# Optimization experiments

Measured on AMD Instinct MI355X. Metric: run time of the kernel, lower is better.

## Reference

```python
import jax, jax.numpy as jnp
import numpy as np

D = 512      # n_embd
H = 8        # n_head
L = 2        # n_layer (per stack)
T = 2048     # sequence length / block_size
B = 1        # batch
BANDS = (999, 9)  # band_width for [phase, tool] stacks
EPS = 1e-5


def _sinusoidal(n_pos, dim):
    pos = np.arange(n_pos)[:, None].astype(np.float64)
    j = np.arange(dim)[None, :]
    angle = pos / np.power(10000.0, 2 * (j // 2) / dim)
    out = np.zeros((n_pos, dim), np.float32)
    out[:, 0::2] = np.sin(angle[:, 0::2])
    out[:, 1::2] = np.cos(angle[:, 1::2])
    return jnp.asarray(out)


def setup_inputs() -> dict:
    key = jax.random.key(0)
    ks = jax.random.split(key, 8)
    s = 0.02
    rn = lambda k, shp: jax.random.normal(k, shp, jnp.float32) * s
    inp = {
        "x": jax.random.normal(ks[0], (B, T, D), jnp.float32),
        "pos_emb": _sinusoidal(T, D),            # sinusoidal, frozen
        # leading dim 2 = [phase stack, tool stack], then layer dim L
        "ln1_w": jnp.ones((2, L, D)), "ln1_b": jnp.zeros((2, L, D)),
        "ln2_w": jnp.ones((2, L, D)), "ln2_b": jnp.zeros((2, L, D)),
        "Wq": rn(ks[1], (2, L, D, D)), "bq": jnp.zeros((2, L, D)),
        "Wk": rn(ks[2], (2, L, D, D)), "bk": jnp.zeros((2, L, D)),
        "Wv": rn(ks[3], (2, L, D, D)), "bv": jnp.zeros((2, L, D)),
        "Wo": rn(ks[4], (2, L, D, D)), "bo": jnp.zeros((2, L, D)),
        "W1": rn(ks[5], (2, L, D, 2 * D)), "b1": jnp.zeros((2, L, 2 * D)),
        "W2": rn(ks[6], (2, L, 2 * D, D)), "b2": jnp.zeros((2, L, D)),
        "lnf_w": jnp.ones((D,)), "lnf_b": jnp.zeros((D,)),
    }
    return inp


def _ln(x, w, b):
    mu = x.mean(-1, keepdims=True)
    var = ((x - mu) ** 2).mean(-1, keepdims=True)
    return (x - mu) / jnp.sqrt(var + EPS) * w + b


def _attn(x, Wq, bq, Wk, bk, Wv, bv, Wo, bo, bw):
    Bx, Tx, _ = x.shape
    Dh = D // H
    heads = lambda W, b: (x @ W + b).reshape(Bx, Tx, H, Dh).transpose(0, 2, 1, 3)
    q, k, v = heads(Wq, bq), heads(Wk, bk), heads(Wv, bv)
    att = jnp.einsum('bhqd,bhkd->bhqk', q, k) / jnp.sqrt(jnp.float32(Dh))
    i = jnp.arange(Tx)[:, None]
    j = jnp.arange(Tx)[None, :]
    mask = (j <= i) & (j >= i - bw)  # causal band
    att = jnp.where(mask, att, -jnp.inf)
    att = jax.nn.softmax(att, axis=-1)
    y = jnp.einsum('bhqk,bhkd->bhqd', att, v).transpose(0, 2, 1, 3).reshape(Bx, Tx, D)
    return y @ Wo + bo


def reference(x, pos_emb, ln1_w, ln1_b, ln2_w, ln2_b,
              Wq, bq, Wk, bk, Wv, bv, Wo, bo,
              W1, b1, W2, b2, lnf_w, lnf_b):
    Tx = x.shape[1]
    h0 = x + pos_emb[None, :Tx]
    outs = []
    for s in range(2):  # phase stack, tool stack
        bw = BANDS[s]
        h = h0
        for l in range(L):
            h = h + _attn(_ln(h, ln1_w[s, l], ln1_b[s, l]),
                          Wq[s, l], bq[s, l], Wk[s, l], bk[s, l],
                          Wv[s, l], bv[s, l], Wo[s, l], bo[s, l], bw)
            hm = _ln(h, ln2_w[s, l], ln2_b[s, l])
            h = h + (jax.nn.gelu(hm @ W1[s, l] + b1[s, l], approximate=False)
                     @ W2[s, l] + b2[s, l])
        outs.append(_ln(h, lnf_w, lnf_b))
    return (outs[0], outs[1])
```

## Files before the change

### kernel.cpp

```cpp
#include <hip/hip_runtime.h>
#include <stdint.h>

#define T 2048
#define D 512
#define NH 8
#define DH 64
#define L 2

typedef float floatx4 __attribute__((ext_vector_type(4)));
typedef short shortx8 __attribute__((ext_vector_type(8)));
typedef unsigned short u16;
typedef unsigned short u16x4 __attribute__((ext_vector_type(4)));

__device__ __forceinline__ u16 f2bf(float f) {
    union { float f; uint32_t u; } c; c.f = f;
    uint32_t u = c.u;
    u += 0x7fffu + ((u >> 16) & 1u);
    return (u16)(u >> 16);
}

__device__ __forceinline__ float bf2f(u16 v) {
    union { uint32_t u; float f; } c; c.u = ((uint32_t)v) << 16;
    return c.f;
}

__device__ __forceinline__ void load_lds16(const void* g, void* l) {
    __builtin_amdgcn_global_load_lds((const __attribute__((address_space(1))) void*)g,
                                     (__attribute__((address_space(3))) void*)l,
                                     16, 0, 0);
}

struct TransJobs {
    const float* src[6];
    u16* dst[6];
    const float* x;
    const float* pos;
    u16* h;
};

__global__ __launch_bounds__(256) void pre_kernel(TransJobs j) {
    __shared__ float tile[32][33];
    int tid = threadIdx.x;
    if (blockIdx.z == 24) {
        int idx = (blockIdx.y * 32 + blockIdx.x) * 256 + tid;
        float4 xv = ((const float4*)j.x)[idx];
        float4 pv = ((const float4*)j.pos)[idx];
        u16x4 hh;
        hh[0] = f2bf(xv.x + pv.x); hh[1] = f2bf(xv.y + pv.y);
        hh[2] = f2bf(xv.z + pv.z); hh[3] = f2bf(xv.w + pv.w);
        ((u16x4*)j.h)[idx] = hh;
        ((u16x4*)j.h)[idx + (T * D / 4)] = hh;
        return;
    }
    int m = blockIdx.z >> 2, slice = blockIdx.z & 3;
    int R = (m == 5) ? 1024 : 512;
    int C = (m == 4) ? 1024 : 512;
    if (blockIdx.x * 32 >= C || blockIdx.y * 32 >= R) return;
    const float* in = j.src[m] + (size_t)slice * R * C;
    u16* out = j.dst[m] + (size_t)slice * R * C;
    int tx = tid & 31, ty = tid >> 5;
    int x = blockIdx.x * 32 + tx;
    int y0 = blockIdx.y * 32;
#pragma unroll
    for (int i = 0; i < 4; i++)
        tile[ty + i * 8][tx] = in[(size_t)(y0 + ty + i * 8) * C + x];
    __syncthreads();
    int ox = y0 + tx;
#pragma unroll
    for (int i = 0; i < 4; i++)
        out[(size_t)(blockIdx.x * 32 + ty + i * 8) * R + ox] = f2bf(tile[tx][ty + i * 8]);
}

__global__ __launch_bounds__(256) void ln_res_kernel(u16* __restrict__ h,
                                                     const u16* __restrict__ part,
                                                     const float* __restrict__ wp,
                                                     const float* __restrict__ bp,
                                                     u16* __restrict__ out, int l) {
    int row = blockIdx.x * 4 + (threadIdx.x >> 6);
    int lane = threadIdx.x & 63;
    int s = row >> 11;
    int c0 = lane * 4;
    u16* xr = h + (size_t)row * D;
    u16x4 h0 = *(const u16x4*)(xr + c0);
    u16x4 h1 = *(const u16x4*)(xr + c0 + 256);
    float4 v0, v1;
    v0.x = bf2f(h0[0]); v0.y = bf2f(h0[1]); v0.z = bf2f(h0[2]); v0.w = bf2f(h0[3]);
    v1.x = bf2f(h1[0]); v1.y = bf2f(h1[1]); v1.z = bf2f(h1[2]); v1.w = bf2f(h1[3]);
    if (part) {
        const u16* p0r = part + (size_t)s * 2 * T * D + (size_t)(row & (T - 1)) * D;
        const u16* p1r = p0r + (size_t)T * D;
        u16x4 a0 = *(const u16x4*)(p0r + c0), a1 = *(const u16x4*)(p0r + c0 + 256);
        u16x4 e0 = *(const u16x4*)(p1r + c0), e1 = *(const u16x4*)(p1r + c0 + 256);
        v0.x += bf2f(a0[0]) + bf2f(e0[0]); v0.y += bf2f(a0[1]) + bf2f(e0[1]);
        v0.z += bf2f(a0[2]) + bf2f(e0[2]); v0.w += bf2f(a0[3]) + bf2f(e0[3]);
        v1.x += bf2f(a1[0]) + bf2f(e1[0]); v1.y += bf2f(a1[1]) + bf2f(e1[1]);
        v1.z += bf2f(a1[2]) + bf2f(e1[2]); v1.w += bf2f(a1[3]) + bf2f(e1[3]);
        u16x4 s0, s1;
        s0[0] = f2bf(v0.x); s0[1] = f2bf(v0.y); s0[2] = f2bf(v0.z); s0[3] = f2bf(v0.w);
        s1[0] = f2bf(v1.x); s1[1] = f2bf(v1.y); s1[2] = f2bf(v1.z); s1[3] = f2bf(v1.w);
        *(u16x4*)(xr + c0) = s0;
        *(u16x4*)(xr + c0 + 256) = s1;
    }
    float sum = v0.x + v0.y + v0.z + v0.w + v1.x + v1.y + v1.z + v1.w;
    float sq = v0.x*v0.x + v0.y*v0.y + v0.z*v0.z + v0.w*v0.w
             + v1.x*v1.x + v1.y*v1.y + v1.z*v1.z + v1.w*v1.w;
#pragma unroll
    for (int d2 = 1; d2 < 64; d2 <<= 1) { sum += __shfl_xor(sum, d2); sq += __shfl_xor(sq, d2); }
    float mu = sum * (1.0f / D);
    float var = sq * (1.0f / D) - mu * mu;
    float rstd = rsqrtf(var + 1e-5f);
    const float* w = wp + (size_t)(s * L + l) * D;
    const float* b = bp + (size_t)(s * L + l) * D;
    u16x4 p0, p1;
#pragma unroll
    for (int jj = 0; jj < 4; jj++) {
        float a = (jj == 0 ? v0.x : jj == 1 ? v0.y : jj == 2 ? v0.z : v0.w);
        p0[jj] = f2bf((a - mu) * rstd * w[c0 + jj] + b[c0 + jj]);
        float c = (jj == 0 ? v1.x : jj == 1 ? v1.y : jj == 2 ? v1.z : v1.w);
        p1[jj] = f2bf((c - mu) * rstd * w[c0 + 256 + jj] + b[c0 + 256 + jj]);
    }
    *(u16x4*)(out + (size_t)row * D + c0) = p0;
    *(u16x4*)(out + (size_t)row * D + c0 + 256) = p1;
}

__global__ __launch_bounds__(256) void lnf_kernel(const u16* __restrict__ h,
                                                  const u16* __restrict__ part,
                                                  const float* __restrict__ w,
                                                  const float* __restrict__ b,
                                                  float* __restrict__ out) {
    int row = blockIdx.x * 4 + (threadIdx.x >> 6);
    int lane = threadIdx.x & 63;
    int s = row >> 11;
    int c0 = lane * 4;
    const u16* xr = h + (size_t)row * D;
    u16x4 h0 = *(const u16x4*)(xr + c0);
    u16x4 h1 = *(const u16x4*)(xr + c0 + 256);
    float4 v0, v1;
    v0.x = bf2f(h0[0]); v0.y = bf2f(h0[1]); v0.z = bf2f(h0[2]); v0.w = bf2f(h0[3]);
    v1.x = bf2f(h1[0]); v1.y = bf2f(h1[1]); v1.z = bf2f(h1[2]); v1.w = bf2f(h1[3]);
    const u16* p0r = part + (size_t)s * 2 * T * D + (size_t)(row & (T - 1)) * D;
    const u16* p1r = p0r + (size_t)T * D;
    u16x4 a0 = *(const u16x4*)(p0r + c0), a1 = *(const u16x4*)(p0r + c0 + 256);
    u16x4 e0 = *(const u16x4*)(p1r + c0), e1 = *(const u16x4*)(p1r + c0 + 256);
    v0.x += bf2f(a0[0]) + bf2f(e0[0]); v0.y += bf2f(a0[1]) + bf2f(e0[1]);
    v0.z += bf2f(a0[2]) + bf2f(e0[2]); v0.w += bf2f(a0[3]) + bf2f(e0[3]);
    v1.x += bf2f(a1[0]) + bf2f(e1[0]); v1.y += bf2f(a1[1]) + bf2f(e1[1]);
    v1.z += bf2f(a1[2]) + bf2f(e1[2]); v1.w += bf2f(a1[3]) + bf2f(e1[3]);
    float sum = v0.x + v0.y + v0.z + v0.w + v1.x + v1.y + v1.z + v1.w;
    float sq = v0.x*v0.x + v0.y*v0.y + v0.z*v0.z + v0.w*v0.w
             + v1.x*v1.x + v1.y*v1.y + v1.z*v1.z + v1.w*v1.w;
#pragma unroll
    for (int d2 = 1; d2 < 64; d2 <<= 1) { sum += __shfl_xor(sum, d2); sq += __shfl_xor(sq, d2); }
    float mu = sum * (1.0f / D);
    float var = sq * (1.0f / D) - mu * mu;
    float rstd = rsqrtf(var + 1e-5f);
    float4 r0, r1;
    r0.x = (v0.x - mu) * rstd * w[c0+0] + b[c0+0];
    r0.y = (v0.y - mu) * rstd * w[c0+1] + b[c0+1];
    r0.z = (v0.z - mu) * rstd * w[c0+2] + b[c0+2];
    r0.w = (v0.w - mu) * rstd * w[c0+3] + b[c0+3];
    r1.x = (v1.x - mu) * rstd * w[c0+256+0] + b[c0+256+0];
    r1.y = (v1.y - mu) * rstd * w[c0+256+1] + b[c0+256+1];
    r1.z = (v1.z - mu) * rstd * w[c0+256+2] + b[c0+256+2];
    r1.w = (v1.w - mu) * rstd * w[c0+256+3] + b[c0+256+3];
    *(float4*)(out + (size_t)row * D + c0) = r0;
    *(float4*)(out + (size_t)row * D + c0 + 256) = r1;
}

struct GemmPtrs {
    const u16* A[6];
    const u16* Bt[6];
    const float* bias[6];
    void* C[6];
};

#define EPI_QKV  0
#define EPI_GELU 1
#define EPI_PART 2

template <int EPI>
__global__ __launch_bounds__(256) void gemm_kernel(GemmPtrs p, int M, int N, int K, int KS) {
    __shared__ __align__(16) u16 lA[2][64 * 32];
    __shared__ __align__(16) u16 lB[2][64 * 32];
    int nchunk = K / KS;
    int pidx = blockIdx.z / nchunk;
    int kc = blockIdx.z % nchunk;
    int koff = kc * KS;
    const u16* A = p.A[pidx];
    const u16* Bt = p.Bt[pidx];
    int m0 = blockIdx.y * 64, n0 = blockIdx.x * 64;
    int tid = threadIdx.x;
    int lane = tid & 63, wave = tid >> 6;
    int wx = wave & 1, wy = wave >> 1;
    int l16 = lane & 15, q4 = lane >> 4;
    const u16* ag = A + (size_t)(m0 + (tid >> 2)) * K + koff + (tid & 3) * 8;
    const u16* bg = Bt + (size_t)(n0 + (tid >> 2)) * K + koff + (tid & 3) * 8;
    floatx4 acc[2][2] = {};
    for (int k0 = 0; k0 < KS; k0 += 64) {
        __syncthreads();
#pragma unroll
        for (int kh = 0; kh < 2; kh++) {
            load_lds16(ag + k0 + kh * 32, &lA[kh][tid * 8]);
            load_lds16(bg + k0 + kh * 32, &lB[kh][tid * 8]);
        }
        __syncthreads();
#pragma unroll
        for (int kh = 0; kh < 2; kh++) {
            shortx8 af[2], bf[2];
#pragma unroll
            for (int t = 0; t < 2; t++) {
                af[t] = *(const shortx8*)(&lA[kh][(wy * 32 + t * 16 + l16) * 32 + q4 * 8]);
                bf[t] = *(const shortx8*)(&lB[kh][(wx * 32 + t * 16 + l16) * 32 + q4 * 8]);
            }
#pragma unroll
            for (int i = 0; i < 2; i++)
#pragma unroll
                for (int j = 0; j < 2; j++)
                    acc[i][j] = __builtin_amdgcn_mfma_f32_16x16x32_bf16(af[i], bf[j], acc[i][j], 0, 0, 0);
        }
    }
    const float* bias = p.bias[pidx];
    bool vtrans = (EPI == EPI_QKV) && (pidx % 3 == 2);
#pragma unroll
    for (int i = 0; i < 2; i++) {
        int row0 = m0 + wy * 32 + i * 16 + q4 * 4;
#pragma unroll
        for (int j = 0; j < 2; j++) {
            int col = n0 + wx * 32 + j * 16 + l16;
            float bz = (kc == 0) ? bias[col] : 0.0f;
            floatx4 a = acc[i][j];
            if (EPI == EPI_QKV) {
                if (vtrans) {
                    u16x4 pk;
#pragma unroll
                    for (int r = 0; r < 4; r++) pk[r] = f2bf(a[r] + bz);
                    *(u16x4*)((u16*)p.C[pidx] + (size_t)col * M + row0) = pk;
                } else {
#pragma unroll
                    for (int r = 0; r < 4; r++)
                        ((u16*)p.C[pidx])[(size_t)(row0 + r) * N + col] = f2bf(a[r] + bz);
                }
            } else if (EPI == EPI_GELU) {
#pragma unroll
                for (int r = 0; r < 4; r++) {
                    float v = a[r] + bz;
                    float g = 0.5f * v * (1.0f + erff(v * 0.70710678118f));
                    ((u16*)p.C[pidx])[(size_t)(row0 + r) * N + col] = f2bf(g);
                }
            } else {
#pragma unroll
                for (int r = 0; r < 4; r++)
                    ((u16*)p.C[pidx])[(size_t)kc * M * N + (size_t)(row0 + r) * N + col] = f2bf(a[r] + bz);
            }
        }
    }
}

__global__ __launch_bounds__(256) void attn_kernel(const u16* __restrict__ qg,
                                                   const u16* __restrict__ kg,
                                                   const u16* __restrict__ vtg,
                                                   u16* __restrict__ ao,
                                                   int bw0, int bw1) {
    __shared__ __align__(16) u16 pbuf[4][16 * 32];
    __shared__ float cl[4][16];
    __shared__ float co[4][16][64];
    int s = blockIdx.z, hh = blockIdx.y, q0 = blockIdx.x * 16;
    int bw = (s == 0) ? bw0 : bw1;
    int tid = threadIdx.x, wave = tid >> 6, lane = tid & 63;
    int l16 = lane & 15, q4 = lane >> 4;
    const u16* Q = qg + (size_t)s * T * D;
    const u16* Kp = kg + (size_t)s * T * D;
    const u16* V = vtg + (size_t)s * D * T;
    int hd = hh * DH;
    shortx8 qf0 = *(const shortx8*)(Q + (size_t)(q0 + l16) * D + hd + q4 * 8);
    shortx8 qf1 = *(const shortx8*)(Q + (size_t)(q0 + l16) * D + hd + 32 + q4 * 8);
    floatx4 o[4] = {};
    float lsum[4] = {};
    int klo = q0 - bw; if (klo < 0) klo = 0; klo &= ~31;
    int khi = q0 + 15;
    u16* pw = pbuf[wave];
    int kt0 = klo + wave * 32;
    shortx8 kf0, kf1, kf2, kf3, vf0, vf1, vf2, vf3;
    if (kt0 <= khi) {
        kf0 = *(const shortx8*)(Kp + (size_t)(kt0 + l16) * D + hd + q4 * 8);
        kf1 = *(const shortx8*)(Kp + (size_t)(kt0 + l16) * D + hd + 32 + q4 * 8);
        kf2 = *(const shortx8*)(Kp + (size_t)(kt0 + 16 + l16) * D + hd + q4 * 8);
        kf3 = *(const shortx8*)(Kp + (size_t)(kt0 + 16 + l16) * D + hd + 32 + q4 * 8);
        vf0 = *(const shortx8*)(V + (size_t)(hd + 0 * 16 + l16) * T + kt0 + q4 * 8);
        vf1 = *(const shortx8*)(V + (size_t)(hd + 1 * 16 + l16) * T + kt0 + q4 * 8);
        vf2 = *(const shortx8*)(V + (size_t)(hd + 2 * 16 + l16) * T + kt0 + q4 * 8);
        vf3 = *(const shortx8*)(V + (size_t)(hd + 3 * 16 + l16) * T + kt0 + q4 * 8);
    }
    for (int kt = kt0; kt <= khi; kt += 128) {
        floatx4 s0 = {}, s1 = {};
        s0 = __builtin_amdgcn_mfma_f32_16x16x32_bf16(qf0, kf0, s0, 0, 0, 0);
        s0 = __builtin_amdgcn_mfma_f32_16x16x32_bf16(qf1, kf1, s0, 0, 0, 0);
        s1 = __builtin_amdgcn_mfma_f32_16x16x32_bf16(qf0, kf2, s1, 0, 0, 0);
        s1 = __builtin_amdgcn_mfma_f32_16x16x32_bf16(qf1, kf3, s1, 0, 0, 0);
        int ktn = kt + 128;
        shortx8 nk0, nk1, nk2, nk3, nv0, nv1, nv2, nv3;
        if (ktn <= khi) {
            nk0 = *(const shortx8*)(Kp + (size_t)(ktn + l16) * D + hd + q4 * 8);
            nk1 = *(const shortx8*)(Kp + (size_t)(ktn + l16) * D + hd + 32 + q4 * 8);
            nk2 = *(const shortx8*)(Kp + (size_t)(ktn + 16 + l16) * D + hd + q4 * 8);
            nk3 = *(const shortx8*)(Kp + (size_t)(ktn + 16 + l16) * D + hd + 32 + q4 * 8);
            nv0 = *(const shortx8*)(V + (size_t)(hd + 0 * 16 + l16) * T + ktn + q4 * 8);
            nv1 = *(const shortx8*)(V + (size_t)(hd + 1 * 16 + l16) * T + ktn + q4 * 8);
            nv2 = *(const shortx8*)(V + (size_t)(hd + 2 * 16 + l16) * T + ktn + q4 * 8);
            nv3 = *(const shortx8*)(V + (size_t)(hd + 3 * 16 + l16) * T + ktn + q4 * 8);
        }
#pragma unroll
        for (int r = 0; r < 4; r++) {
            int row = q0 + q4 * 4 + r;
            int c0 = kt + l16, c1 = kt + 16 + l16;
            float p0 = (c0 <= row && c0 >= row - bw) ? __expf(s0[r] * 0.125f) : 0.0f;
            float p1 = (c1 <= row && c1 >= row - bw) ? __expf(s1[r] * 0.125f) : 0.0f;
            lsum[r] += p0 + p1;
            pw[(q4 * 4 + r) * 32 + l16] = f2bf(p0);
            pw[(q4 * 4 + r) * 32 + 16 + l16] = f2bf(p1);
        }
        shortx8 pf = *(const shortx8*)(pw + l16 * 32 + q4 * 8);
        o[0] = __builtin_amdgcn_mfma_f32_16x16x32_bf16(pf, vf0, o[0], 0, 0, 0);
        o[1] = __builtin_amdgcn_mfma_f32_16x16x32_bf16(pf, vf1, o[1], 0, 0, 0);
        o[2] = __builtin_amdgcn_mfma_f32_16x16x32_bf16(pf, vf2, o[2], 0, 0, 0);
        o[3] = __builtin_amdgcn_mfma_f32_16x16x32_bf16(pf, vf3, o[3], 0, 0, 0);
        kf0 = nk0; kf1 = nk1; kf2 = nk2; kf3 = nk3;
        vf0 = nv0; vf1 = nv1; vf2 = nv2; vf3 = nv3;
    }
#pragma unroll
    for (int r = 0; r < 4; r++) {
#pragma unroll
        for (int d2 = 1; d2 < 16; d2 <<= 1) lsum[r] += __shfl_xor(lsum[r], d2);
    }
    if (l16 == 0) {
#pragma unroll
        for (int r = 0; r < 4; r++) cl[wave][q4 * 4 + r] = lsum[r];
    }
#pragma unroll
    for (int n = 0; n < 4; n++)
#pragma unroll
        for (int r = 0; r < 4; r++)
            co[wave][q4 * 4 + r][n * 16 + l16] = o[n][r];
    __syncthreads();
#pragma unroll
    for (int i = 0; i < 4; i++) {
        int idx = tid + i * 256;
        int row = idx >> 6, col = idx & 63;
        float Ls = cl[0][row] + cl[1][row] + cl[2][row] + cl[3][row];
        float O = co[0][row][col] + co[1][row][col] + co[2][row][col] + co[3][row][col];
        ao[(size_t)s * T * D + (size_t)(q0 + row) * D + hd + col] = f2bf(O / Ls);
    }
}

extern "C" void kernel_launch(void* const* d_in, const int* in_sizes, int n_in,
                              void* d_out, int out_size, void* d_ws, size_t ws_size,
                              hipStream_t stream) {
    (void)in_sizes; (void)n_in; (void)out_size; (void)ws_size;
    const float* x     = (const float*)d_in[0];
    const float* pos   = (const float*)d_in[1];
    const float* ln1_w = (const float*)d_in[2];
    const float* ln1_b = (const float*)d_in[3];
    const float* ln2_w = (const float*)d_in[4];
    const float* ln2_b = (const float*)d_in[5];
    const float* Wq    = (const float*)d_in[6];
    const float* bq    = (const float*)d_in[7];
    const float* Wk    = (const float*)d_in[8];
    const float* bk    = (const float*)d_in[9];
    const float* Wv    = (const float*)d_in[10];
    const float* bv    = (const float*)d_in[11];
    const float* Wo    = (const float*)d_in[12];
    const float* bo    = (const float*)d_in[13];
    const float* W1    = (const float*)d_in[14];
    const float* b1    = (const float*)d_in[15];
    const float* W2    = (const float*)d_in[16];
    const float* b2    = (const float*)d_in[17];
    const float* lnf_w = (const float*)d_in[18];
    const float* lnf_b = (const float*)d_in[19];

    char* ws = (char*)d_ws;
    size_t off = 0;
    auto alloc = [&](size_t bytes) { void* p = ws + off; off += (bytes + 255) & ~(size_t)255; return p; };
    u16* WqT = (u16*)alloc((size_t)4 * 512 * 512 * 2);
    u16* WkT = (u16*)alloc((size_t)4 * 512 * 512 * 2);
    u16* WvT = (u16*)alloc((size_t)4 * 512 * 512 * 2);
    u16* WoT = (u16*)alloc((size_t)4 * 512 * 512 * 2);
    u16* W1T = (u16*)alloc((size_t)4 * 512 * 1024 * 2);
    u16* W2T = (u16*)alloc((size_t)4 * 1024 * 512 * 2);
    u16* h   = (u16*)alloc((size_t)2 * T * D * 2);
    u16* xln = (u16*)alloc((size_t)2 * T * D * 2);
    u16* qb  = (u16*)alloc((size_t)2 * T * D * 2);
    u16* kb  = (u16*)alloc((size_t)2 * T * D * 2);
    u16* vt  = (u16*)alloc((size_t)2 * T * D * 2);
    u16* ao  = (u16*)alloc((size_t)2 * T * D * 2);
    u16* ff  = (u16*)alloc((size_t)2 * T * 1024 * 2);
    u16* pp = (u16*)alloc((size_t)2 * 2 * T * D * 2);
    u16* pf = (u16*)alloc((size_t)2 * 2 * T * D * 2);

    TransJobs tj;
    tj.src[0] = Wq; tj.dst[0] = WqT;
    tj.src[1] = Wk; tj.dst[1] = WkT;
    tj.src[2] = Wv; tj.dst[2] = WvT;
    tj.src[3] = Wo; tj.dst[3] = WoT;
    tj.src[4] = W1; tj.dst[4] = W1T;
    tj.src[5] = W2; tj.dst[5] = W2T;
    tj.x = x; tj.pos = pos; tj.h = h;
    pre_kernel<<<dim3(32, 32, 25), 256, 0, stream>>>(tj);

    for (int l = 0; l < L; l++) {
        ln_res_kernel<<<(2 * T) / 4, 256, 0, stream>>>(h, l == 0 ? nullptr : pf,
                                                       ln1_w, ln1_b, xln, l);

        GemmPtrs g{};
        for (int s = 0; s < 2; s++) {
            int wo = s * L + l;
            const u16* a = xln + (size_t)s * T * D;
            g.A[s * 3 + 0] = a; g.Bt[s * 3 + 0] = WqT + (size_t)wo * 512 * 512;
            g.bias[s * 3 + 0] = bq + (size_t)wo * 512; g.C[s * 3 + 0] = qb + (size_t)s * T * D;
            g.A[s * 3 + 1] = a; g.Bt[s * 3 + 1] = WkT + (size_t)wo * 512 * 512;
            g.bias[s * 3 + 1] = bk + (size_t)wo * 512; g.C[s * 3 + 1] = kb + (size_t)s * T * D;
            g.A[s * 3 + 2] = a; g.Bt[s * 3 + 2] = WvT + (size_t)wo * 512 * 512;
            g.bias[s * 3 + 2] = bv + (size_t)wo * 512; g.C[s * 3 + 2] = vt + (size_t)s * T * D;
        }
        gemm_kernel<EPI_QKV><<<dim3(8, 32, 6), 256, 0, stream>>>(g, T, 512, 512, 512);

        attn_kernel<<<dim3(128, 8, 2), 256, 0, stream>>>(qb, kb, vt, ao, 999, 9);

        GemmPtrs gp{};
        for (int s = 0; s < 2; s++) {
            int wo = s * L + l;
            gp.A[s] = ao + (size_t)s * T * D;
            gp.Bt[s] = WoT + (size_t)wo * 512 * 512;
            gp.bias[s] = bo + (size_t)wo * 512;
            gp.C[s] = pp + (size_t)s * 2 * T * D;
        }
        gemm_kernel<EPI_PART><<<dim3(8, 32, 4), 256, 0, stream>>>(gp, T, 512, 512, 256);

        ln_res_kernel<<<(2 * T) / 4, 256, 0, stream>>>(h, pp, ln2_w, ln2_b, xln, l);

        GemmPtrs g1{};
        for (int s = 0; s < 2; s++) {
            int wo = s * L + l;
            g1.A[s] = xln + (size_t)s * T * D;
            g1.Bt[s] = W1T + (size_t)wo * 512 * 1024;
            g1.bias[s] = b1 + (size_t)wo * 1024;
            g1.C[s] = ff + (size_t)s * T * 1024;
        }
        gemm_kernel<EPI_GELU><<<dim3(16, 32, 2), 256, 0, stream>>>(g1, T, 1024, 512, 512);

        GemmPtrs g2{};
        for (int s = 0; s < 2; s++) {
            int wo = s * L + l;
            g2.A[s] = ff + (size_t)s * T * 1024;
            g2.Bt[s] = W2T + (size_t)wo * 1024 * 512;
            g2.bias[s] = b2 + (size_t)wo * 512;
            g2.C[s] = pf + (size_t)s * 2 * T * D;
        }
        gemm_kernel<EPI_PART><<<dim3(8, 32, 4), 256, 0, stream>>>(g2, T, 512, 1024, 512);
    }

    lnf_kernel<<<(2 * T) / 4, 256, 0, stream>>>(h, pf, lnf_w, lnf_b, (float*)d_out);
}
```

Before: 319.8 us.

## Give each wave private LDS tiles and prefetch next K chunk without block barriers

The GEMM loop now has each wave load its own 32x64 slices of A and B into a private LDS region, instead of sharing one block-wide tile. This removes both __syncthreads per K step and replaces them with explicit vmcnt/lgkmcnt waits. Once the fragments are in registers, the next chunk's global-to-LDS loads are issued before the MFMAs, so memory traffic overlaps compute. In exchange, A and B rows are loaded redundantly across waves (each row is fetched by two waves), which raises global/L2 traffic and doubles LDS use.

```diff
diff --git a/kernel.cpp b/kernel.cpp
--- a/kernel.cpp
+++ b/kernel.cpp
@@ -29,6 +29,9 @@
                                      (__attribute__((address_space(3))) void*)l,
                                      16, 0, 0);
 }
+
+#define WAIT_VM0   __builtin_amdgcn_s_waitcnt(0x0F70)
+#define WAIT_LGKM0 __builtin_amdgcn_s_waitcnt(0xC07F)
 
 struct TransJobs {
     const float* src[6];
@@ -180,8 +183,7 @@
 
 template <int EPI>
 __global__ __launch_bounds__(256) void gemm_kernel(GemmPtrs p, int M, int N, int K, int KS) {
-    __shared__ __align__(16) u16 lA[2][64 * 32];
-    __shared__ __align__(16) u16 lB[2][64 * 32];
+    __shared__ __align__(16) u16 smem[4][4096];
     int nchunk = K / KS;
     int pidx = blockIdx.z / nchunk;
     int kc = blockIdx.z % nchunk;
@@ -193,31 +195,45 @@
     int lane = tid & 63, wave = tid >> 6;
     int wx = wave & 1, wy = wave >> 1;
     int l16 = lane & 15, q4 = lane >> 4;
-    const u16* ag = A + (size_t)(m0 + (tid >> 2)) * K + koff + (tid & 3) * 8;
-    const u16* bg = Bt + (size_t)(n0 + (tid >> 2)) * K + koff + (tid & 3) * 8;
+    u16* ldsA = smem[wave];
+    u16* ldsB = smem[wave] + 2048;
+    int arow0 = m0 + wy * 32, brow0 = n0 + wx * 32;
+    const u16* agl = A + (size_t)(arow0 + (lane >> 3)) * K + koff + (lane & 7) * 8;
+    const u16* bgl = Bt + (size_t)(brow0 + (lane >> 3)) * K + koff + (lane & 7) * 8;
+    size_t r8 = (size_t)8 * K;
     floatx4 acc[2][2] = {};
-    for (int k0 = 0; k0 < KS; k0 += 64) {
-        __syncthreads();
-#pragma unroll
-        for (int kh = 0; kh < 2; kh++) {
-            load_lds16(ag + k0 + kh * 32, &lA[kh][tid * 8]);
-            load_lds16(bg + k0 + kh * 32, &lB[kh][tid * 8]);
-        }
-        __syncthreads();
-#pragma unroll
-        for (int kh = 0; kh < 2; kh++) {
-            shortx8 af[2], bf[2];
-#pragma unroll
-            for (int t = 0; t < 2; t++) {
-                af[t] = *(const shortx8*)(&lA[kh][(wy * 32 + t * 16 + l16) * 32 + q4 * 8]);
-                bf[t] = *(const shortx8*)(&lB[kh][(wx * 32 + t * 16 + l16) * 32 + q4 * 8]);
+#pragma unroll
+    for (int g = 0; g < 4; g++) {
+        load_lds16(agl + g * r8, ldsA + g * 512 + lane * 8);
+        load_lds16(bgl + g * r8, ldsB + g * 512 + lane * 8);
+    }
+    int nch = KS / 64;
+    for (int c = 0; c < nch; c++) {
+        WAIT_VM0;
+        shortx8 af[2][2], bf[2][2];
+#pragma unroll
+        for (int t = 0; t < 2; t++)
+#pragma unroll
+            for (int kh = 0; kh < 2; kh++) {
+                af[t][kh] = *(const shortx8*)(ldsA + (t * 16 + l16) * 64 + kh * 32 + q4 * 8);
+                bf[t][kh] = *(const shortx8*)(ldsB + (t * 16 + l16) * 64 + kh * 32 + q4 * 8);
             }
+        WAIT_LGKM0;
+        if (c + 1 < nch) {
+            int k0 = (c + 1) * 64;
+#pragma unroll
+            for (int g = 0; g < 4; g++) {
+                load_lds16(agl + g * r8 + k0, ldsA + g * 512 + lane * 8);
+                load_lds16(bgl + g * r8 + k0, ldsB + g * 512 + lane * 8);
+            }
+        }
+#pragma unroll
+        for (int kh = 0; kh < 2; kh++)
 #pragma unroll
             for (int i = 0; i < 2; i++)
 #pragma unroll
                 for (int j = 0; j < 2; j++)
-                    acc[i][j] = __builtin_amdgcn_mfma_f32_16x16x32_bf16(af[i], bf[j], acc[i][j], 0, 0, 0);
-        }
+                    acc[i][j] = __builtin_amdgcn_mfma_f32_16x16x32_bf16(af[i][kh], bf[j][kh], acc[i][j], 0, 0, 0);
     }
     const float* bias = p.bias[pidx];
     bool vtrans = (EPI == EPI_QKV) && (pidx % 3 == 2);
```

Result: slower. 331.8 us (+3.8%).
